# Optimization experiments

Hardware: AMD Instinct MI355X
Metric: run time of the kernel (lower is better)

## Reference

```python
import jax, jax.numpy as jnp
import numpy as np

CAPACITY = 0.75      # MoDRouter capacity
ACT_STEPS = 3        # act_max_steps
EPS = 0.01           # ACT halting epsilon
PONDER = 0.01        # act_ponder_cost


def setup_inputs() -> dict:
    key = jax.random.key(0)
    k1, k2, k3 = jax.random.split(key, 3)
    x = jax.random.normal(k1, (4, 8192, 1024), dtype=jnp.float32)
    router_w = jax.random.normal(k2, (1024,), dtype=jnp.float32) * 0.02  # nn.Linear(dim,1,bias=False), std=0.02
    halt_w = jax.random.normal(k3, (1024,), dtype=jnp.float32) * 0.02    # halt linear weight (zeros-init in src; perturbed for nontrivial signal)
    halt_b = -jnp.ones((1,), dtype=jnp.float32)                          # halt bias init -1.0
    return {"x": x, "router_w": router_w, "halt_w": halt_w, "halt_b": halt_b}


def _mod_step(x, router_w):
    """MoDRouter.forward + identity block + MoDRouter.scatter_back."""
    b, s, d = x.shape
    k = max(1, int(s * CAPACITY))
    scores = jnp.einsum('bsd,d->bs', x, router_w)                 # (b, s)
    topk_scores, idx = jax.lax.top_k(scores, k)                   # sorted desc, like torch.topk
    routed = jnp.take_along_axis(x, idx[:, :, None], axis=1)      # (b, k, d) gather
    processed = routed                                            # identity stand-in for Block (undefined in source)
    w = jax.nn.softmax(topk_scores, axis=1)[:, :, None]           # straight-through weights (b, k, 1)
    new_vals = processed * w + (1.0 - w) * routed                 # weighted_processed + (1-w)*original_at_indices
    return x.at[jnp.arange(b)[:, None], idx].set(new_vals)        # scatter back; unrouted tokens = identity


def _act_combine(states, halt_w, halt_b):
    """ACTHaltingUnit.forward: masked accumulation over recurrence steps."""
    b, s, d = states[0].shape
    dt = states[0].dtype
    acc = jnp.zeros((b, s), dt)
    out = jnp.zeros((b, s, d), dt)
    rem = jnp.ones((b, s), dt)
    n_upd = jnp.zeros((b, s), dt)
    for state in states:  # fixed small loop over recurrence steps
        h = jax.nn.sigmoid(jnp.einsum('bsd,d->bs', state, halt_w) + halt_b[0])
        still = (acc < 1.0 - EPS).astype(dt)
        new_acc = acc + h * still
        use_rem = (new_acc > 1.0 - EPS).astype(dt) * still
        use_h = (1.0 - use_rem) * still
        p = use_h * h + use_rem * rem
        out = out + p[:, :, None] * state
        acc = acc + p * still
        rem = rem - p * still
        n_upd = n_upd + still
    ponder_loss = PONDER * jnp.mean(n_upd)
    return out, ponder_loss


def reference(x, router_w, halt_w, halt_b):
    states = []
    cur = x
    for _ in range(ACT_STEPS):
        cur = _mod_step(cur, router_w)
        states.append(cur)
    return _act_combine(states, halt_w, halt_b)
```

## Files before the change

kernel.cpp:

```cpp
#include <hip/hip_runtime.h>
#include <math.h>

#define N_TOKENS 32768
#define DIM      1024
#define WAVES_PER_BLOCK 4
#define TOK_PER_WAVE 8

typedef float v4f __attribute__((ext_vector_type(4)));

__global__ void modgpt_init(int* __restrict__ n_acc) {
    if (threadIdx.x == 0 && blockIdx.x == 0) n_acc[0] = 0;
}

__global__ __launch_bounds__(256) void modgpt_main(
        const float* __restrict__ x,
        const float* __restrict__ halt_w,
        const float* __restrict__ halt_b,
        float* __restrict__ out,
        int* __restrict__ n_acc) {
    const int wave = threadIdx.x >> 6;
    const int lane = threadIdx.x & 63;
    const int token0 = (blockIdx.x * WAVES_PER_BLOCK + wave) * TOK_PER_WAVE;

    const v4f* __restrict__ xin = (const v4f*)(x + (size_t)token0 * DIM);
    v4f* __restrict__ oout      = (v4f*)(out + (size_t)token0 * DIM);
    const v4f* __restrict__ w4  = (const v4f*)halt_w;

    const v4f w0 = w4[lane];
    const v4f w1 = w4[lane + 64];
    const v4f w2 = w4[lane + 128];
    const v4f w3 = w4[lane + 192];
    const float hb = halt_b[0];

    int n_sum = 0;

    v4f c0 = xin[lane];
    v4f c1 = xin[lane + 64];
    v4f c2 = xin[lane + 128];
    v4f c3 = xin[lane + 192];

    #pragma unroll
    for (int t = 0; t < TOK_PER_WAVE; ++t) {
        v4f p0, p1, p2, p3;
        if (t + 1 < TOK_PER_WAVE) {
            const v4f* nx = xin + (size_t)(t + 1) * 256;
            p0 = nx[lane];
            p1 = nx[lane + 64];
            p2 = nx[lane + 128];
            p3 = nx[lane + 192];
        }

        v4f m = c0 * w0 + c1 * w1 + c2 * w2 + c3 * w3;
        float dot = m.x + m.y + m.z + m.w;
        #pragma unroll
        for (int off = 32; off >= 1; off >>= 1)
            dot += __shfl_xor(dot, off, 64);

        const float h = 1.0f / (1.0f + expf(-(dot + hb)));

        float acc = 0.0f, rem = 1.0f, P = 0.0f;
        int n = 0;
        #pragma unroll
        for (int s = 0; s < 3; ++s) {
            if (acc < 0.99f) {
                const float na = acc + h;
                const float p  = (na > 0.99f) ? rem : h;
                P   += p;
                acc += p;
                rem -= p;
                n   += 1;
            }
        }
        n_sum += n;

        v4f* op = oout + (size_t)t * 256;
        __builtin_nontemporal_store(c0 * P, op + lane);
        __builtin_nontemporal_store(c1 * P, op + lane + 64);
        __builtin_nontemporal_store(c2 * P, op + lane + 128);
        __builtin_nontemporal_store(c3 * P, op + lane + 192);

        c0 = p0; c1 = p1; c2 = p2; c3 = p3;
    }

    __shared__ int sn[WAVES_PER_BLOCK];
    if (lane == 0) sn[wave] = n_sum;
    __syncthreads();
    if (threadIdx.x == 0)
        atomicAdd(n_acc, sn[0] + sn[1] + sn[2] + sn[3]);
}

__global__ void modgpt_finalize(const int* __restrict__ n_acc,
                                float* __restrict__ ponder_out) {
    if (threadIdx.x == 0 && blockIdx.x == 0)
        ponder_out[0] = 0.01f * ((float)n_acc[0] / (float)N_TOKENS);
}

extern "C" void kernel_launch(void* const* d_in, const int* in_sizes, int n_in,
                              void* d_out, int out_size, void* d_ws, size_t ws_size,
                              hipStream_t stream) {
    const float* x        = (const float*)d_in[0];
    const float* halt_w   = (const float*)d_in[2];
    const float* halt_b   = (const float*)d_in[3];
    float* out            = (float*)d_out;
    int*   n_acc          = (int*)d_ws;

    modgpt_init<<<1, 64, 0, stream>>>(n_acc);
    modgpt_main<<<N_TOKENS / (WAVES_PER_BLOCK * TOK_PER_WAVE), 256, 0, stream>>>(
        x, halt_w, halt_b, out, n_acc);
    modgpt_finalize<<<1, 64, 0, stream>>>(n_acc, out + (size_t)N_TOKENS * DIM);
}
```

Before: 241.8 us.

## Process one token per wave and spread ponder counter over strided slots

Each wave now handles a single token instead of eight with software prefetch, so the grid grows eightfold for more memory-level parallelism. The global halting-step counter is split into 64 cache-line-strided slots, and a wave shuffle reduces them in the finalize kernel, to limit atomic contention from the larger block count. The cost is more blocks, more atomics and more per-block setup such as reloading the halt weights, and the prefetch pipelining is lost.

```diff
diff --git a/kernel.cpp b/kernel.cpp
--- a/kernel.cpp
+++ b/kernel.cpp
@@ -3,13 +3,14 @@
 
 #define N_TOKENS 32768
 #define DIM      1024
-#define WAVES_PER_BLOCK 4
-#define TOK_PER_WAVE 8
+#define N_SLOTS  64
+#define SLOT_STRIDE 32
 
 typedef float v4f __attribute__((ext_vector_type(4)));
 
 __global__ void modgpt_init(int* __restrict__ n_acc) {
-    if (threadIdx.x == 0 && blockIdx.x == 0) n_acc[0] = 0;
+    if (blockIdx.x == 0 && threadIdx.x < N_SLOTS)
+        n_acc[threadIdx.x * SLOT_STRIDE] = 0;
 }
 
 __global__ __launch_bounds__(256) void modgpt_main(
@@ -20,11 +21,16 @@
         int* __restrict__ n_acc) {
     const int wave = threadIdx.x >> 6;
     const int lane = threadIdx.x & 63;
-    const int token0 = (blockIdx.x * WAVES_PER_BLOCK + wave) * TOK_PER_WAVE;
+    const int token = blockIdx.x * 4 + wave;
 
-    const v4f* __restrict__ xin = (const v4f*)(x + (size_t)token0 * DIM);
-    v4f* __restrict__ oout      = (v4f*)(out + (size_t)token0 * DIM);
+    const v4f* __restrict__ xin = (const v4f*)(x + (size_t)token * DIM);
+    v4f* __restrict__ op        = (v4f*)(out + (size_t)token * DIM);
     const v4f* __restrict__ w4  = (const v4f*)halt_w;
+
+    const v4f c0 = xin[lane];
+    const v4f c1 = xin[lane + 64];
+    const v4f c2 = xin[lane + 128];
+    const v4f c3 = xin[lane + 192];
 
     const v4f w0 = w4[lane];
     const v4f w1 = w4[lane + 64];
@@ -32,67 +38,49 @@
     const v4f w3 = w4[lane + 192];
     const float hb = halt_b[0];
 
-    int n_sum = 0;
+    v4f m = c0 * w0 + c1 * w1 + c2 * w2 + c3 * w3;
+    float dot = m.x + m.y + m.z + m.w;
+    #pragma unroll
+    for (int off = 32; off >= 1; off >>= 1)
+        dot += __shfl_xor(dot, off, 64);
 
-    v4f c0 = xin[lane];
-    v4f c1 = xin[lane + 64];
-    v4f c2 = xin[lane + 128];
-    v4f c3 = xin[lane + 192];
+    const float h = 1.0f / (1.0f + expf(-(dot + hb)));
 
+    float acc = 0.0f, rem = 1.0f, P = 0.0f;
+    int n = 0;
     #pragma unroll
-    for (int t = 0; t < TOK_PER_WAVE; ++t) {
-        v4f p0, p1, p2, p3;
-        if (t + 1 < TOK_PER_WAVE) {
-            const v4f* nx = xin + (size_t)(t + 1) * 256;
-            p0 = nx[lane];
-            p1 = nx[lane + 64];
-            p2 = nx[lane + 128];
-            p3 = nx[lane + 192];
+    for (int s = 0; s < 3; ++s) {
+        if (acc < 0.99f) {
+            const float na = acc + h;
+            const float p  = (na > 0.99f) ? rem : h;
+            P   += p;
+            acc += p;
+            rem -= p;
+            n   += 1;
         }
-
-        v4f m = c0 * w0 + c1 * w1 + c2 * w2 + c3 * w3;
-        float dot = m.x + m.y + m.z + m.w;
-        #pragma unroll
-        for (int off = 32; off >= 1; off >>= 1)
-            dot += __shfl_xor(dot, off, 64);
-
-        const float h = 1.0f / (1.0f + expf(-(dot + hb)));
-
-        float acc = 0.0f, rem = 1.0f, P = 0.0f;
-        int n = 0;
-        #pragma unroll
-        for (int s = 0; s < 3; ++s) {
-            if (acc < 0.99f) {
-                const float na = acc + h;
-                const float p  = (na > 0.99f) ? rem : h;
-                P   += p;
-                acc += p;
-                rem -= p;
-                n   += 1;
-            }
-        }
-        n_sum += n;
-
-        v4f* op = oout + (size_t)t * 256;
-        __builtin_nontemporal_store(c0 * P, op + lane);
-        __builtin_nontemporal_store(c1 * P, op + lane + 64);
-        __builtin_nontemporal_store(c2 * P, op + lane + 128);
-        __builtin_nontemporal_store(c3 * P, op + lane + 192);
-
-        c0 = p0; c1 = p1; c2 = p2; c3 = p3;
     }
 
-    __shared__ int sn[WAVES_PER_BLOCK];
-    if (lane == 0) sn[wave] = n_sum;
+    __builtin_nontemporal_store(c0 * P, op + lane);
+    __builtin_nontemporal_store(c1 * P, op + lane + 64);
+    __builtin_nontemporal_store(c2 * P, op + lane + 128);
+    __builtin_nontemporal_store(c3 * P, op + lane + 192);
+
+    __shared__ int sn[4];
+    if (lane == 0) sn[wave] = n;
     __syncthreads();
     if (threadIdx.x == 0)
-        atomicAdd(n_acc, sn[0] + sn[1] + sn[2] + sn[3]);
+        atomicAdd(n_acc + (blockIdx.x & (N_SLOTS - 1)) * SLOT_STRIDE,
+                  sn[0] + sn[1] + sn[2] + sn[3]);
 }
 
 __global__ void modgpt_finalize(const int* __restrict__ n_acc,
                                 float* __restrict__ ponder_out) {
-    if (threadIdx.x == 0 && blockIdx.x == 0)
-        ponder_out[0] = 0.01f * ((float)n_acc[0] / (float)N_TOKENS);
+    int v = n_acc[(threadIdx.x & 63) * SLOT_STRIDE];
+    #pragma unroll
+    for (int off = 32; off >= 1; off >>= 1)
+        v += __shfl_xor(v, off, 64);
+    if (threadIdx.x == 0)
+        ponder_out[0] = 0.01f * ((float)v / (float)N_TOKENS);
 }
 
 extern "C" void kernel_launch(void* const* d_in, const int* in_sizes, int n_in,
@@ -105,7 +93,6 @@
     int*   n_acc          = (int*)d_ws;
 
     modgpt_init<<<1, 64, 0, stream>>>(n_acc);
-    modgpt_main<<<N_TOKENS / (WAVES_PER_BLOCK * TOK_PER_WAVE), 256, 0, stream>>>(
-        x, halt_w, halt_b, out, n_acc);
+    modgpt_main<<<N_TOKENS / 4, 256, 0, stream>>>(x, halt_w, halt_b, out, n_acc);
     modgpt_finalize<<<1, 64, 0, stream>>>(n_acc, out + (size_t)N_TOKENS * DIM);
 }
```

Result: no change. 238.3 us (-1.5%).
